# Performance work log

Measured on AMD Instinct MI355X. Metric: run time of the kernel, lower is better.

## Reference

```python
import jax, jax.numpy as jnp
import numpy as np

B, H, S, D = 4, 16, 4096, 64

def setup_inputs() -> dict:
    key = jax.random.key(0)
    kq, kk, kv = jax.random.split(key, 3)
    q = jax.random.normal(kq, (B, H, S, D), dtype=jnp.float32)
    k = jax.random.normal(kk, (B, H, S, D), dtype=jnp.float32)
    v = jax.random.normal(kv, (B, H, S, D), dtype=jnp.float32)
    return {"q": q, "k": k, "v": v}

def reference(q, k, v):
    # Original: (q @ k^T) @ v with score [B,H,S,S].
    # Mathematically identical reassociation: q @ (k^T @ v),
    # state kv has shape [B,H,D,D] -> avoids the SxS intermediate.
    kv = jnp.einsum('bhsd,bhse->bhde', k, v)  # [B,H,D,D]
    out = jnp.einsum('bhsd,bhde->bhse', q, kv)  # [B,H,S,D]
    return out
```

## Files before the change

kernel.cpp:

```cpp
#include <hip/hip_runtime.h>

#define BH  64
#define SEQ 4096
#define DH  64
#define NCHUNK 32
#define CROWS  (SEQ / NCHUNK)

typedef __attribute__((ext_vector_type(8))) short bf16x8v;
typedef __attribute__((ext_vector_type(4))) float f32x4v;

__device__ __forceinline__ short f2bf(float x) {
  unsigned u = __float_as_uint(x);
  return (short)((u + 0x7FFFu + ((u >> 16) & 1u)) >> 16);
}

__global__ __launch_bounds__(256) void kv_partial_kernel(
    const float* __restrict__ k, const float* __restrict__ v,
    float* __restrict__ partial) {
  const int t = threadIdx.x;
  const int bh = blockIdx.x >> 5;
  const int chunk = blockIdx.x & (NCHUNK - 1);
  const int l  = t & 63;
  const int w  = t >> 6;
  const int lg = l >> 4;
  const int ln = l & 15;

  const size_t rowbase = (size_t)bh * SEQ * DH + ((size_t)chunk * CROWS + w * 32) * DH;
  const float* kb = k + rowbase;
  const float* vb = v + rowbase;

  __shared__ float smem[8192];

  float kf[32], vf[32];
#pragma unroll
  for (int j = 0; j < 8; ++j) {
    const float* kr = kb + (size_t)(lg * 8 + j) * DH;
    const float* vr = vb + (size_t)(lg * 8 + j) * DH;
#pragma unroll
    for (int m = 0; m < 4; ++m) {
      kf[m * 8 + j] = kr[m * 16 + ln];
      vf[m * 8 + j] = vr[m * 16 + ln];
    }
  }

  bf16x8v a[4], b[4];
#pragma unroll
  for (int m = 0; m < 4; ++m)
#pragma unroll
    for (int j = 0; j < 8; ++j) {
      a[m][j] = f2bf(kf[m * 8 + j]);
      b[m][j] = f2bf(vf[m * 8 + j]);
    }

  f32x4v acc[4][4];
#pragma unroll
  for (int m = 0; m < 4; ++m)
#pragma unroll
    for (int n = 0; n < 4; ++n) {
      acc[m][n] = (f32x4v){0.f, 0.f, 0.f, 0.f};
      acc[m][n] = __builtin_amdgcn_mfma_f32_16x16x32_bf16(
          a[m], b[n], acc[m][n], 0, 0, 0);
    }

  if (w >= 2) {
    float* reg = smem + (w - 2) * 4096;
#pragma unroll
    for (int m = 0; m < 4; ++m)
#pragma unroll
      for (int n = 0; n < 4; ++n) {
        float4 x = {acc[m][n][0], acc[m][n][1], acc[m][n][2], acc[m][n][3]};
        *(float4*)&reg[(m * 4 + n) * 256 + l * 4] = x;
      }
  }
  __syncthreads();
  if (w < 2) {
    const float* reg = smem + w * 4096;
#pragma unroll
    for (int m = 0; m < 4; ++m)
#pragma unroll
      for (int n = 0; n < 4; ++n) {
        float4 x = *(const float4*)&reg[(m * 4 + n) * 256 + l * 4];
        acc[m][n][0] += x.x; acc[m][n][1] += x.y;
        acc[m][n][2] += x.z; acc[m][n][3] += x.w;
      }
  }
  __syncthreads();
  if (w == 1) {
#pragma unroll
    for (int m = 0; m < 4; ++m)
#pragma unroll
      for (int n = 0; n < 4; ++n) {
        float4 x = {acc[m][n][0], acc[m][n][1], acc[m][n][2], acc[m][n][3]};
        *(float4*)&smem[(m * 4 + n) * 256 + l * 4] = x;
      }
  }
  __syncthreads();
  if (w == 0) {
    float* pb = partial + (size_t)blockIdx.x * (DH * DH);
#pragma unroll
    for (int m = 0; m < 4; ++m)
#pragma unroll
      for (int n = 0; n < 4; ++n) {
        float4 x = *(const float4*)&smem[(m * 4 + n) * 256 + l * 4];
        acc[m][n][0] += x.x; acc[m][n][1] += x.y;
        acc[m][n][2] += x.z; acc[m][n][3] += x.w;
#pragma unroll
        for (int r = 0; r < 4; ++r)
          pb[(m * 16 + lg * 4 + r) * 64 + n * 16 + ln] = acc[m][n][r];
      }
  }
}

__global__ __launch_bounds__(256) void kv_reduce_kernel(
    const float* __restrict__ partial, float* __restrict__ kvf) {
  const int gid = blockIdx.x * 256 + threadIdx.x;
  const int bh = gid >> 10;
  const int idx = gid & 1023;
  float4 s = {0.f, 0.f, 0.f, 0.f};
  for (int c = 0; c < NCHUNK; ++c) {
    const float4* p = (const float4*)(partial + ((size_t)bh * NCHUNK + c) * (DH * DH));
    float4 x = p[idx];
    s.x += x.x; s.y += x.y; s.z += x.z; s.w += x.w;
  }
  ((float4*)kvf)[gid] = s;
}

__global__ __launch_bounds__(256) void out_kernel(
    const float* __restrict__ q, const float* __restrict__ kvf,
    float* __restrict__ out) {
  const int t = threadIdx.x;
  const int bh = blockIdx.x >> 6;
  const int rb = blockIdx.x & 63;
  const int row = rb * 64 + (t >> 2);
  const int c0 = (t & 3) * 16;

  __shared__ float kv_lds[64 * 64];

  const float4* gkv4 = (const float4*)(kvf + (size_t)bh * (DH * DH));
  float4* kv4 = (float4*)kv_lds;
#pragma unroll
  for (int j = 0; j < 4; ++j) kv4[t + j * 256] = gkv4[t + j * 256];

  const float* qrow = q + (size_t)bh * SEQ * DH + (size_t)row * DH;
  float4 qv[16];
#pragma unroll
  for (int i = 0; i < 16; ++i) qv[i] = *(const float4*)&qrow[i * 4];

  __syncthreads();

  float acc[16];
#pragma unroll
  for (int j = 0; j < 16; ++j) acc[j] = 0.f;

#pragma unroll
  for (int dc = 0; dc < 16; ++dc) {
    float qs[4] = {qv[dc].x, qv[dc].y, qv[dc].z, qv[dc].w};
#pragma unroll
    for (int dd = 0; dd < 4; ++dd) {
      const float* kr = &kv_lds[(dc * 4 + dd) * 64 + c0];
      float4 k0 = *(const float4*)&kr[0];
      float4 k1 = *(const float4*)&kr[4];
      float4 k2 = *(const float4*)&kr[8];
      float4 k3 = *(const float4*)&kr[12];
      const float qsv = qs[dd];
      acc[0]  += qsv * k0.x; acc[1]  += qsv * k0.y;
      acc[2]  += qsv * k0.z; acc[3]  += qsv * k0.w;
      acc[4]  += qsv * k1.x; acc[5]  += qsv * k1.y;
      acc[6]  += qsv * k1.z; acc[7]  += qsv * k1.w;
      acc[8]  += qsv * k2.x; acc[9]  += qsv * k2.y;
      acc[10] += qsv * k2.z; acc[11] += qsv * k2.w;
      acc[12] += qsv * k3.x; acc[13] += qsv * k3.y;
      acc[14] += qsv * k3.z; acc[15] += qsv * k3.w;
    }
  }

  float* ob = out + (size_t)bh * SEQ * DH + (size_t)row * DH + c0;
#pragma unroll
  for (int j = 0; j < 4; ++j) {
    float4 w = {acc[4 * j + 0], acc[4 * j + 1], acc[4 * j + 2], acc[4 * j + 3]};
    *(float4*)&ob[4 * j] = w;
  }
}

extern "C" void kernel_launch(void* const* d_in, const int* in_sizes, int n_in,
                              void* d_out, int out_size, void* d_ws, size_t ws_size,
                              hipStream_t stream) {
  const float* q = (const float*)d_in[0];
  const float* k = (const float*)d_in[1];
  const float* v = (const float*)d_in[2];
  float* out = (float*)d_out;

  float* kvf = (float*)d_ws;
  float* partial = kvf + (size_t)BH * DH * DH;

  hipLaunchKernelGGL(kv_partial_kernel, dim3(BH * NCHUNK), dim3(256), 0, stream,
                     k, v, partial);
  hipLaunchKernelGGL(kv_reduce_kernel, dim3(256), dim3(256), 0, stream,
                     partial, kvf);
  hipLaunchKernelGGL(out_kernel, dim3(BH * 64), dim3(256), 0, stream,
                     q, kvf, out);
}
```

Before: 83.23 us.

## Process four K/V steps per wave with double-buffered loads, fewer chunks

Cuts the chunk count from 32 to 8, so each wave now accumulates four 32-row steps instead of one. Register double-buffering with sched_barriers overlaps the next step's global loads with the current step's MFMAs. This shrinks the partial buffer and the reduce kernel's work and spreads the per-block LDS reduction over more rows. The cost is fewer blocks (512) and higher register pressure, which the launch bounds of 2 blocks per SM try to contain.

```diff
diff --git a/kernel.cpp b/kernel.cpp
--- a/kernel.cpp
+++ b/kernel.cpp
@@ -3,7 +3,7 @@
 #define BH  64
 #define SEQ 4096
 #define DH  64
-#define NCHUNK 32
+#define NCHUNK 8
 #define CROWS  (SEQ / NCHUNK)
 
 typedef __attribute__((ext_vector_type(8))) short bf16x8v;
@@ -14,53 +14,80 @@
   return (short)((u + 0x7FFFu + ((u >> 16) & 1u)) >> 16);
 }
 
-__global__ __launch_bounds__(256) void kv_partial_kernel(
+#define LOADSTEP(kf, vf, step)                                              \
+  do {                                                                      \
+    const float* kp_ = kb + (size_t)(step) * 32 * DH;                       \
+    const float* vp_ = vb + (size_t)(step) * 32 * DH;                       \
+    _Pragma("unroll")                                                       \
+    for (int j = 0; j < 8; ++j) {                                           \
+      _Pragma("unroll")                                                     \
+      for (int m = 0; m < 4; ++m) {                                         \
+        kf[m * 8 + j] = kp_[(size_t)(lg * 8 + j) * DH + m * 16 + ln];       \
+        vf[m * 8 + j] = vp_[(size_t)(lg * 8 + j) * DH + m * 16 + ln];       \
+      }                                                                     \
+    }                                                                       \
+  } while (0)
+
+#define COMPUTESTEP(kf, vf)                                                 \
+  do {                                                                      \
+    bf16x8v a_[4], b_[4];                                                   \
+    _Pragma("unroll")                                                       \
+    for (int m = 0; m < 4; ++m) {                                           \
+      _Pragma("unroll")                                                     \
+      for (int j = 0; j < 8; ++j) {                                         \
+        a_[m][j] = f2bf(kf[m * 8 + j]);                                     \
+        b_[m][j] = f2bf(vf[m * 8 + j]);                                     \
+      }                                                                     \
+    }                                                                       \
+    _Pragma("unroll")                                                       \
+    for (int m = 0; m < 4; ++m) {                                           \
+      _Pragma("unroll")                                                     \
+      for (int n = 0; n < 4; ++n)                                           \
+        acc[m][n] = __builtin_amdgcn_mfma_f32_16x16x32_bf16(                \
+            a_[m], b_[n], acc[m][n], 0, 0, 0);                              \
+    }                                                                       \
+  } while (0)
+
+__global__ __launch_bounds__(256, 2) void kv_partial_kernel(
     const float* __restrict__ k, const float* __restrict__ v,
     float* __restrict__ partial) {
   const int t = threadIdx.x;
-  const int bh = blockIdx.x >> 5;
+  const int bh = blockIdx.x >> 3;
   const int chunk = blockIdx.x & (NCHUNK - 1);
   const int l  = t & 63;
   const int w  = t >> 6;
   const int lg = l >> 4;
   const int ln = l & 15;
 
-  const size_t rowbase = (size_t)bh * SEQ * DH + ((size_t)chunk * CROWS + w * 32) * DH;
+  const size_t rowbase =
+      (size_t)bh * SEQ * DH + ((size_t)chunk * CROWS + w * 128) * DH;
   const float* kb = k + rowbase;
   const float* vb = v + rowbase;
 
   __shared__ float smem[8192];
 
-  float kf[32], vf[32];
-#pragma unroll
-  for (int j = 0; j < 8; ++j) {
-    const float* kr = kb + (size_t)(lg * 8 + j) * DH;
-    const float* vr = vb + (size_t)(lg * 8 + j) * DH;
-#pragma unroll
-    for (int m = 0; m < 4; ++m) {
-      kf[m * 8 + j] = kr[m * 16 + ln];
-      vf[m * 8 + j] = vr[m * 16 + ln];
-    }
-  }
-
-  bf16x8v a[4], b[4];
+  f32x4v acc[4][4];
 #pragma unroll
   for (int m = 0; m < 4; ++m)
 #pragma unroll
-    for (int j = 0; j < 8; ++j) {
-      a[m][j] = f2bf(kf[m * 8 + j]);
-      b[m][j] = f2bf(vf[m * 8 + j]);
-    }
-
-  f32x4v acc[4][4];
-#pragma unroll
-  for (int m = 0; m < 4; ++m)
-#pragma unroll
-    for (int n = 0; n < 4; ++n) {
-      acc[m][n] = (f32x4v){0.f, 0.f, 0.f, 0.f};
-      acc[m][n] = __builtin_amdgcn_mfma_f32_16x16x32_bf16(
-          a[m], b[n], acc[m][n], 0, 0, 0);
-    }
+    for (int n = 0; n < 4; ++n) acc[m][n] = (f32x4v){0.f, 0.f, 0.f, 0.f};
+
+  float kA[32], vA[32], kB[32], vB[32];
+
+  LOADSTEP(kA, vA, 0);
+  LOADSTEP(kB, vB, 1);
+  __builtin_amdgcn_sched_barrier(0);
+  COMPUTESTEP(kA, vA);
+  __builtin_amdgcn_sched_barrier(0);
+  LOADSTEP(kA, vA, 2);
+  __builtin_amdgcn_sched_barrier(0);
+  COMPUTESTEP(kB, vB);
+  __builtin_amdgcn_sched_barrier(0);
+  LOADSTEP(kB, vB, 3);
+  __builtin_amdgcn_sched_barrier(0);
+  COMPUTESTEP(kA, vA);
+  __builtin_amdgcn_sched_barrier(0);
+  COMPUTESTEP(kB, vB);
 
   if (w >= 2) {
     float* reg = smem + (w - 2) * 4096;
```

New measurement: 76.75 us. -7.8%, faster.
